# Optimization experiments

Measured on AMD Instinct MI355X. Metric: run time of the kernel, lower is better.

The kernel has to match this reference:

```python
import jax, jax.numpy as jnp
import numpy as np

VOCAB = 32000
EMBED = 512
HIDDEN = 1024
BATCH = 16
SEQ = 256


def setup_inputs() -> dict:
    key = jax.random.key(0)
    ks = jax.random.split(key, 12)
    E, H, V = EMBED, HIDDEN, VOCAB
    s_gate = 1.0 / np.sqrt(E + H)
    s_out = 1.0 / np.sqrt(H)
    return {
        "input": jax.random.randint(ks[0], (BATCH, SEQ), 0, V, dtype=jnp.int32),
        "embed": jax.random.normal(ks[1], (V, E), dtype=jnp.float32),
        "W_f": jax.random.normal(ks[2], (E + H, H), dtype=jnp.float32) * s_gate,
        "b_f": jax.random.normal(ks[3], (H,), dtype=jnp.float32) * s_gate,
        "W_i": jax.random.normal(ks[4], (E + H, H), dtype=jnp.float32) * s_gate,
        "b_i": jax.random.normal(ks[5], (H,), dtype=jnp.float32) * s_gate,
        "W_c": jax.random.normal(ks[6], (E + H, H), dtype=jnp.float32) * s_gate,
        "b_c": jax.random.normal(ks[7], (H,), dtype=jnp.float32) * s_gate,
        "W_o": jax.random.normal(ks[8], (E + H, H), dtype=jnp.float32) * s_gate,
        "b_o": jax.random.normal(ks[9], (H,), dtype=jnp.float32) * s_gate,
        "W_out": jax.random.normal(ks[10], (H, V), dtype=jnp.float32) * s_out,
        "b_out": jax.random.normal(ks[11], (V,), dtype=jnp.float32) * s_out,
    }


def reference(input, embed, W_f, b_f, W_i, b_i, W_c, b_c, W_o, b_o, W_out, b_out):
    B = input.shape[0]
    H = W_f.shape[1]
    tokens = embed[input]                     # [B, S, E]
    xs = jnp.swapaxes(tokens, 0, 1)           # [S, B, E] for scan over time

    def step(carry, x_t):
        h, c = carry
        catted = jnp.concatenate([x_t, h], axis=1)   # [B, E+H]
        f = jax.nn.sigmoid(catted @ W_f + b_f)
        i = jax.nn.sigmoid(catted @ W_i + b_i)
        cand = jnp.tanh(catted @ W_c + b_c)
        o = jax.nn.sigmoid(catted @ W_o + b_o)
        c = c * f + cand * i
        h = c * o
        return (h, c), h

    h0 = jnp.zeros((B, H), dtype=tokens.dtype)
    c0 = jnp.zeros((B, H), dtype=tokens.dtype)
    _, hs = jax.lax.scan(step, (h0, c0), xs)  # hs: [S, B, H]
    hiddens = jnp.swapaxes(hs, 0, 1)          # [B, S, H]
    return hiddens @ W_out + b_out            # [B, S, V]
```

## Files before the change

kernel.cpp:

```cpp
#include <hip/hip_runtime.h>
#include <hip/hip_bf16.h>

#define VOCAB  32000
#define EMBED  512
#define HIDDEN 1024
#define BATCH  16
#define SEQ    256
#define NROW   (BATCH*SEQ)
#define GCOLS  (4*HIDDEN)
#define NWREC  64
#define NWPACK 192
#define NTILE  8000
#define SENT32 0xFFFFFFFFu

typedef unsigned short u16;
typedef unsigned int   u32;
typedef unsigned long long u64;
typedef __attribute__((ext_vector_type(4))) float f32x4;
typedef __attribute__((ext_vector_type(8))) short bf16x8;
typedef __attribute__((ext_vector_type(8))) unsigned short u16x8;
typedef __attribute__((ext_vector_type(2))) unsigned long long u64x2;

__device__ inline u16 f2bf(float f){
  __hip_bfloat16 h = __float2bfloat16(f);
  return __builtin_bit_cast(u16, h);
}
__device__ inline void gload_lds16(const void* g, void* l){
  __builtin_amdgcn_global_load_lds((const __attribute__((address_space(1))) u32*)g,
                                   (__attribute__((address_space(3))) u32*)l, 16, 0, 0);
}
__device__ __forceinline__ u32 al32(const u32* p){
  return __hip_atomic_load(p, __ATOMIC_RELAXED, __HIP_MEMORY_SCOPE_AGENT);
}
__device__ __forceinline__ u64 al64(const u64* p){
  return __hip_atomic_load(p, __ATOMIC_RELAXED, __HIP_MEMORY_SCOPE_AGENT);
}
__device__ __forceinline__ void as32(u32* p, u32 v){
  __hip_atomic_store(p, v, __ATOMIC_RELAXED, __HIP_MEMORY_SCOPE_AGENT);
}
__device__ __forceinline__ void as64(u64* p, u64 v){
  __hip_atomic_store(p, v, __ATOMIC_RELAXED, __HIP_MEMORY_SCOPE_AGENT);
}

__global__ __launch_bounds__(256) void pack_gates(
    const float* __restrict__ Wf, const float* __restrict__ Wi,
    const float* __restrict__ Wc, const float* __restrict__ Wo,
    const float* __restrict__ bf_, const float* __restrict__ bi_,
    const float* __restrict__ bc_, const float* __restrict__ bo_,
    u16* __restrict__ Wxp, u16* __restrict__ Whp, float* __restrict__ bcat)
{
  const int NT_WX = (GCOLS/16)*(EMBED/32)*64;
  const int NT_WH = (GCOLS/16)*(HIDDEN/32)*64;
  int t = blockIdx.x*256 + threadIdx.x;
  if (t < NT_WX){
    int u = t;
    int lane = u&63; int kb = (u>>6)&15; int nblk = u>>10;
    int col = nblk*16 + (lane&15);
    int k0  = kb*32 + ((lane>>4)<<3);
    int g = col>>10, j = col&1023;
    const float* W = (g==0)?Wf:(g==1)?Wi:(g==2)?Wc:Wo;
    u16x8 v;
    #pragma unroll
    for (int e=0;e<8;e++) v[e] = f2bf(W[(size_t)(k0+e)*HIDDEN + j]);
    *(u16x8*)(Wxp + (size_t)u*8) = v;
  } else if (t < NT_WX + NT_WH){
    int u = t - NT_WX;
    int lane = u&63; int kb = (u>>6)&31; int nblk = u>>11;
    int col = nblk*16 + (lane&15);
    int k0  = kb*32 + ((lane>>4)<<3);
    int g = col>>10, j = col&1023;
    const float* W = (g==0)?Wf:(g==1)?Wi:(g==2)?Wc:Wo;
    u16x8 v;
    #pragma unroll
    for (int e=0;e<8;e++) v[e] = f2bf(W[(size_t)(EMBED + k0+e)*HIDDEN + j]);
    *(u16x8*)(Whp + (size_t)u*8) = v;
  } else {
    int u = t - NT_WX - NT_WH;
    if (u < GCOLS){
      int g = u>>10, j = u&1023;
      const float* B = (g==0)?bf_:(g==1)?bi_:(g==2)?bc_:bo_;
      bcat[u] = B[j];
    }
  }
}

__global__ __launch_bounds__(256) void gather_kernel(
    const int* __restrict__ tok, const float* __restrict__ embed, u16* __restrict__ Xg)
{
  int t = blockIdx.x*256 + threadIdx.x;
  int lane = t&63; int kb = (t>>6)&15; int mblk = t>>10;
  int s = mblk; int b = lane&15;
  int token = tok[b*SEQ + s];
  int k0 = kb*32 + ((lane>>4)<<3);
  const float* src = embed + (size_t)token*EMBED + k0;
  u16x8 v;
  #pragma unroll
  for (int e=0;e<8;e++) v[e] = f2bf(src[e]);
  *(u16x8*)(Xg + (size_t)t*8) = v;
}

template<int KB, bool REMAP>
__global__ __launch_bounds__(256,2) void gemm_pk(
    const u16* __restrict__ Ap, const u16* __restrict__ Bp,
    const float* __restrict__ bias, float* __restrict__ C,
    int Nblk128, int N)
{
  __shared__ u16 sm[8192];
  int tid = threadIdx.x; int lane = tid&63; int wv = tid>>6;
  int nwg = gridDim.x;
  int bid = blockIdx.x;
  int swz = (bid&7)*(nwg>>3) + (bid>>3);
  int bm = swz / Nblk128, bn = swz % Nblk128;
  int wr = wv>>1, wc = wv&1;
  f32x4 acc[4][4] = {};
  const u16* Abase = Ap + (size_t)(bm*8)*KB*512;
  const u16* Bbase = Bp + (size_t)(bn*8)*KB*512;
  for (int kb=0; kb<KB; ++kb){
    __syncthreads();
    #pragma unroll
    for (int c2=0;c2<4;c2++){
      int chunk = wv*4 + c2;
      const u16* g;
      if (chunk < 8) g = Abase + ((size_t)chunk*KB + kb)*512 + lane*8;
      else           g = Bbase + ((size_t)(chunk-8)*KB + kb)*512 + lane*8;
      gload_lds16(g, sm + chunk*512);
    }
    __syncthreads();
    bf16x8 a[4], b[4];
    #pragma unroll
    for (int m=0;m<4;m++) a[m] = *(const bf16x8*)(sm + (wr*4+m)*512 + lane*8);
    #pragma unroll
    for (int n=0;n<4;n++) b[n] = *(const bf16x8*)(sm + 4096 + (wc*4+n)*512 + lane*8);
    #pragma unroll
    for (int m=0;m<4;m++)
      #pragma unroll
      for (int n=0;n<4;n++)
        acc[m][n] = __builtin_amdgcn_mfma_f32_16x16x32_bf16(a[m], b[n], acc[m][n], 0,0,0);
  }
  int colb = bn*128 + wc*64;
  int rowb = bm*128 + wr*64;
  #pragma unroll
  for (int m=0;m<4;m++){
    int row0 = rowb + m*16 + (lane>>4)*4;
    #pragma unroll
    for (int n=0;n<4;n++){
      int col = colb + n*16 + (lane&15);
      float bv = bias[col];
      #pragma unroll
      for (int r2=0;r2<4;r2++){
        int row = row0 + r2;
        int orow = REMAP ? ((row&15)*SEQ + (row>>4)) : row;
        C[(size_t)orow*N + col] = acc[m][n][r2] + bv;
      }
    }
  }
}

__global__ __launch_bounds__(256,1) void lstm_fused(
    const u16* __restrict__ Whp, const float* __restrict__ Xpre,
    u16* hb, u16* Hp, u32* cnt, u32* tix, u32* packdone,
    const float* __restrict__ Wout, u16* __restrict__ Woutp,
    const float* __restrict__ bout, float* __restrict__ out)
{
  __shared__ char SMEM[148480];
  __shared__ u32 s_tick;
  u16* smWf = (u16*)SMEM;
  float (*gl)[16][17] = (float (*)[16][17])(SMEM + 131072);
  u16* smg = (u16*)SMEM;

  int tid = threadIdx.x; int lane = tid&63; int v = tid>>6;
  int w = blockIdx.x;

  if (w >= NWREC){
    const int NPK = (VOCAB/16)*(HIDDEN/32)*64;
    int u0 = (w - NWREC)*256 + tid;
    for (int u = u0; u < NPK; u += NWPACK*256){
      int l = u&63; int kb = (u>>6)&31; int nblk = u>>11;
      int col = nblk*16 + (l&15);
      int k0  = kb*32 + ((l>>4)<<3);
      u16x8 vv;
      #pragma unroll
      for (int e=0;e<8;e++) vv[e] = f2bf(Wout[(size_t)(k0+e)*VOCAB + col]);
      u64x2 t2 = __builtin_bit_cast(u64x2, vv);
      u64* dst = (u64*)(Woutp + (size_t)u*8);
      as64(dst+0, t2[0]);
      as64(dst+1, t2[1]);
    }
    asm volatile("s_waitcnt vmcnt(0)" ::: "memory");
    __syncthreads();
    if (tid==0) (void)__hip_atomic_fetch_add(packdone, 1u,
                       __ATOMIC_RELAXED, __HIP_MEMORY_SCOPE_AGENT);
  } else {
    #pragma unroll
    for (int f=0; f<32; ++f){
      int frag = v*32 + f;
      int g = frag>>5, kc = frag&31;
      const u16* src = Whp + ((size_t)(g*64 + w)*32 + kc)*512 + lane*8;
      gload_lds16(src, smWf + (size_t)frag*512);
    }
    asm volatile("s_waitcnt vmcnt(0)" ::: "memory");
    __syncthreads();

    float c = 0.f;
    int pb = tid>>4, pj = tid&15;
    int j = w*16 + pj;
    const int a_row = lane&15, a_k = (lane>>4)*8;
    const float* xb0 = Xpre + (size_t)pb*GCOLS + j;
    float x0 = xb0[0], x1 = xb0[1024], x2 = xb0[2048], x3 = xb0[3072];

    for (int s=0;s<SEQ;s++){
      const u16* rbuf = hb + (size_t)s*16384;
      u64 vv[16];
      for(;;){
        #pragma unroll
        for (int i=0;i<16;i++){
          const u64* p = (const u64*)(rbuf + a_row*1024 + (v*8+(i>>1))*32 + a_k) + (i&1);
          vv[i] = al64(p);
        }
        bool ok = true;
        #pragma unroll
        for (int i=0;i<16;i++)
          ok &= ((u32)vv[i]!=SENT32) & ((u32)(vv[i]>>32)!=SENT32);
        if (ok) break;
        __builtin_amdgcn_s_sleep(1);
      }
      bf16x8 af[8];
      #pragma unroll
      for (int i=0;i<8;i++){
        u64x2 t2 = {vv[2*i], vv[2*i+1]};
        af[i] = __builtin_bit_cast(bf16x8, t2);
      }
      f32x4 acc[4] = {};
      #pragma unroll
      for (int i=0;i<8;i++){
        #pragma unroll
        for (int g=0;g<4;g++){
          bf16x8 wfv = *(const bf16x8*)(smWf + ((size_t)(g*32 + v*8 + i))*512 + lane*8);
          acc[g] = __builtin_amdgcn_mfma_f32_16x16x32_bf16(af[i], wfv, acc[g], 0,0,0);
        }
      }
      {
        int jj = lane&15, b0 = (lane>>4)*4;
        #pragma unroll
        for (int g=0;g<4;g++)
          #pragma unroll
          for (int r2=0;r2<4;r2++)
            gl[v*4+g][b0+r2][jj] = acc[g][r2];
      }
      asm volatile("s_waitcnt lgkmcnt(0)" ::: "memory");
      __builtin_amdgcn_s_barrier();
      __builtin_amdgcn_sched_barrier(0);
      float xn0=0.f,xn1=0.f,xn2=0.f,xn3=0.f;
      if (s < SEQ-1){
        const float* xn = Xpre + ((size_t)(s+1)*16 + pb)*GCOLS + j;
        xn0 = xn[0]; xn1 = xn[1024]; xn2 = xn[2048]; xn3 = xn[3072];
      }
      float p0 = x0 + gl[0][pb][pj] + gl[4][pb][pj] + gl[ 8][pb][pj] + gl[12][pb][pj];
      float p1 = x1 + gl[1][pb][pj] + gl[5][pb][pj] + gl[ 9][pb][pj] + gl[13][pb][pj];
      float p2 = x2 + gl[2][pb][pj] + gl[6][pb][pj] + gl[10][pb][pj] + gl[14][pb][pj];
      float p3 = x3 + gl[3][pb][pj] + gl[7][pb][pj] + gl[11][pb][pj] + gl[15][pb][pj];
      float fg = 1.f/(1.f+__expf(-p0));
      float ig = 1.f/(1.f+__expf(-p1));
      float e2 = __expf(2.f*fminf(fmaxf(p2,-15.f),15.f));
      float cand = (e2-1.f)/(e2+1.f);
      float og = 1.f/(1.f+__expf(-p3));
      c = c*fg + cand*ig;
      float h = c*og;
      x0 = xn0; x1 = xn1; x2 = xn2; x3 = xn3;
      u32 hw_ = (u32)f2bf(h);
      u32 ow_ = (u32)__shfl_xor((int)hw_, 1);
      if ((pj&1)==0){
        u32 word = hw_ | (ow_<<16);
        if (s < SEQ-1){
          u16* wstep = hb + (size_t)(s+1)*16384;
          as32((u32*)wstep + (size_t)pb*512 + w*8 + (pj>>1), word);
        }
        as32((u32*)Hp + (size_t)s*8192 + (size_t)(j>>5)*256
                      + (size_t)(((j>>3)&3)*16 + pb)*4 + ((j&7)>>1), word);
      }
      __builtin_amdgcn_s_barrier();
      __builtin_amdgcn_sched_barrier(0);
      if ((s&7)==7){
        asm volatile("s_waitcnt vmcnt(0)" ::: "memory");
        __builtin_amdgcn_s_barrier();
        asm volatile("" ::: "memory");
        if (tid==0)
          (void)__hip_atomic_fetch_add(cnt + (size_t)(s>>3)*16, 1u,
                   __ATOMIC_RELAXED, __HIP_MEMORY_SCOPE_AGENT);
      }
    }
  }

  if (tid==0){
    while (al32(packdone) < (u32)NWPACK) __builtin_amdgcn_s_sleep(2);
  }
  __syncthreads();

  int wv = tid>>6;
  int wr = wv>>1, wc = wv&1;
  for(;;){
    __syncthreads();
    if (tid==0) s_tick = __hip_atomic_fetch_add(tix, 1u,
                   __ATOMIC_RELAXED, __HIP_MEMORY_SCOPE_AGENT);
    __syncthreads();
    u32 t = s_tick;
    if (t >= (u32)NTILE) break;
    int bm = (int)(t/250u), bn = (int)(t%250u);
    if (tid==0){
      while (al32(cnt + (size_t)bm*16) < (u32)NWREC)
        __builtin_amdgcn_s_sleep(2);
    }
    __syncthreads();
    const u16* Ab = Hp + (size_t)(bm*8)*32*512;
    const u16* Bb = Woutp + (size_t)(bn*8)*32*512;
    auto stage = [&](int kb, int bi){
      #pragma unroll
      for (int c2=0;c2<4;c2++){
        int chunk = wv*4 + c2;
        const u16* g;
        if (chunk < 8) g = Ab + ((size_t)chunk*32 + kb)*512 + lane*8;
        else           g = Bb + ((size_t)(chunk-8)*32 + kb)*512 + lane*8;
        gload_lds16(g, smg + (size_t)bi*8192 + chunk*512);
      }
    };
    stage(0,0); stage(1,1);
    f32x4 acc[4][4] = {};
    for (int kb=0; kb<32; ++kb){
      if (kb<31) asm volatile("s_waitcnt vmcnt(4)" ::: "memory");
      else       asm volatile("s_waitcnt vmcnt(0)" ::: "memory");
      __builtin_amdgcn_s_barrier();
      if (kb+2<32) stage(kb+2, (kb+2)%3);
      const u16* bufp = smg + (size_t)(kb%3)*8192;
      bf16x8 a[4], b[4];
      #pragma unroll
      for (int m=0;m<4;m++) a[m] = *(const bf16x8*)(bufp + (wr*4+m)*512 + lane*8);
      #pragma unroll
      for (int n=0;n<4;n++) b[n] = *(const bf16x8*)(bufp + 4096 + (wc*4+n)*512 + lane*8);
      #pragma unroll
      for (int m=0;m<4;m++)
        #pragma unroll
        for (int n=0;n<4;n++)
          acc[m][n] = __builtin_amdgcn_mfma_f32_16x16x32_bf16(a[m], b[n], acc[m][n], 0,0,0);
    }
    int colb = bn*128 + wc*64;
    int rowb = bm*128 + wr*64;
    #pragma unroll
    for (int m=0;m<4;m++){
      int row0 = rowb + m*16 + (lane>>4)*4;
      #pragma unroll
      for (int n=0;n<4;n++){
        int col = colb + n*16 + (lane&15);
        float bv = bout[col];
        #pragma unroll
        for (int r2=0;r2<4;r2++){
          int row = row0 + r2;
          int orow = (row&15)*SEQ + (row>>4);
          __builtin_nontemporal_store(acc[m][n][r2] + bv,
                                      &out[(size_t)orow*VOCAB + col]);
        }
      }
    }
  }
}

extern "C" void kernel_launch(void* const* d_in, const int* in_sizes, int n_in,
                              void* d_out, int out_size, void* d_ws, size_t ws_size,
                              hipStream_t stream)
{
  (void)in_sizes; (void)n_in; (void)out_size; (void)ws_size;
  const int*   tok   = (const int*)d_in[0];
  const float* embed = (const float*)d_in[1];
  const float* Wf    = (const float*)d_in[2];
  const float* bf_   = (const float*)d_in[3];
  const float* Wi    = (const float*)d_in[4];
  const float* bi_   = (const float*)d_in[5];
  const float* Wc    = (const float*)d_in[6];
  const float* bc_   = (const float*)d_in[7];
  const float* Wo    = (const float*)d_in[8];
  const float* bo_   = (const float*)d_in[9];
  const float* Wout  = (const float*)d_in[10];
  const float* bout  = (const float*)d_in[11];
  float* out = (float*)d_out;

  char* ws = (char*)d_ws;
  size_t off = 0;
  auto alloc = [&](size_t bytes)->void*{
    void* p = ws + off; off += (bytes + 255) & ~(size_t)255; return p;
  };
  u16*  Wxp   = (u16*)alloc((size_t)2097152*2);
  u16*  Xg    = (u16*)alloc((size_t)2097152*2);
  float* bcat = (float*)alloc((size_t)4096*4);
  u16*  hb    = (u16*)ws;
  u16*  Whp   = (u16*)alloc((size_t)4194304*2);
  u16*  Woutp = (u16*)alloc((size_t)32768000*2);
  float* Xpre = (float*)alloc((size_t)NROW*GCOLS*4);
  u16*  Hp    = (u16*)alloc((size_t)4194304*2);
  u32*  cnt   = (u32*)alloc((size_t)4096);
  u32*  tix   = (u32*)alloc((size_t)256);
  u32*  packdone = (u32*)alloc((size_t)256);

  pack_gates<<<3088, 256, 0, stream>>>(Wf,Wi,Wc,Wo, bf_,bi_,bc_,bo_,
                                       Wxp, Whp, bcat);
  gather_kernel<<<1024, 256, 0, stream>>>(tok, embed, Xg);
  gemm_pk<16,false><<<1024, 256, 0, stream>>>(Xg, Wxp, bcat, Xpre, 32, GCOLS);
  (void)hipMemsetAsync(hb, 0x00, 32768, stream);
  (void)hipMemsetAsync((char*)hb + 32768, 0xFF, 255*32768, stream);
  (void)hipMemsetAsync(cnt, 0, 4096 + 256 + 256, stream);
  lstm_fused<<<NWREC+NWPACK, 256, 0, stream>>>(Whp, Xpre, hb, Hp, cnt, tix,
                                               packdone, Wout, Woutp, bout, out);
}
```

Before: 1.169 ms.

## Statically assign output column blocks to worker CTAs and overlap projection with recurrence

Worker CTAs now each own a fixed set of output column tiles (two or one of 250). Each packs only its own Wout slice to bf16 and then computes projection tiles for every row block as soon as the recurrence signals that block done. This removes the global packdone barrier and the atomic ticket dispenser, and the recurrent CTAs no longer join the output GEMM. The projection can overlap with the LSTM recurrence and packed weights are reused locally. The risks are load imbalance between workers with 2 and 1 tiles, and losing the 64 recurrent CTAs as GEMM workers after the recurrence ends.

```diff
diff --git a/kernel.cpp b/kernel.cpp
--- a/kernel.cpp
+++ b/kernel.cpp
@@ -9,8 +9,7 @@
 #define NROW   (BATCH*SEQ)
 #define GCOLS  (4*HIDDEN)
 #define NWREC  64
-#define NWPACK 192
-#define NTILE  8000
+#define NWORK  192
 #define SENT32 0xFFFFFFFFu
 
 typedef unsigned short u16;
@@ -36,9 +35,6 @@
   return __hip_atomic_load(p, __ATOMIC_RELAXED, __HIP_MEMORY_SCOPE_AGENT);
 }
 __device__ __forceinline__ void as32(u32* p, u32 v){
-  __hip_atomic_store(p, v, __ATOMIC_RELAXED, __HIP_MEMORY_SCOPE_AGENT);
-}
-__device__ __forceinline__ void as64(u64* p, u64 v){
   __hip_atomic_store(p, v, __ATOMIC_RELAXED, __HIP_MEMORY_SCOPE_AGENT);
 }
 
@@ -158,12 +154,11 @@
 
 __global__ __launch_bounds__(256,1) void lstm_fused(
     const u16* __restrict__ Whp, const float* __restrict__ Xpre,
-    u16* hb, u16* Hp, u32* cnt, u32* tix, u32* packdone,
+    u16* hb, u16* Hp, u32* cnt,
     const float* __restrict__ Wout, u16* __restrict__ Woutp,
     const float* __restrict__ bout, float* __restrict__ out)
 {
   __shared__ char SMEM[148480];
-  __shared__ u32 s_tick;
   u16* smWf = (u16*)SMEM;
   float (*gl)[16][17] = (float (*)[16][17])(SMEM + 131072);
   u16* smg = (u16*)SMEM;
@@ -172,24 +167,88 @@
   int w = blockIdx.x;
 
   if (w >= NWREC){
-    const int NPK = (VOCAB/16)*(HIDDEN/32)*64;
-    int u0 = (w - NWREC)*256 + tid;
-    for (int u = u0; u < NPK; u += NWPACK*256){
-      int l = u&63; int kb = (u>>6)&31; int nblk = u>>11;
-      int col = nblk*16 + (l&15);
-      int k0  = kb*32 + ((l>>4)<<3);
-      u16x8 vv;
-      #pragma unroll
-      for (int e=0;e<8;e++) vv[e] = f2bf(Wout[(size_t)(k0+e)*VOCAB + col]);
-      u64x2 t2 = __builtin_bit_cast(u64x2, vv);
-      u64* dst = (u64*)(Woutp + (size_t)u*8);
-      as64(dst+0, t2[0]);
-      as64(dst+1, t2[1]);
+    int wkr = w - NWREC;
+    int bn0, nbn;
+    if (wkr < 58){ bn0 = wkr*2;          nbn = 2; }
+    else         { bn0 = 116 + (wkr-58); nbn = 1; }
+    for (int q=0; q<nbn; ++q){
+      int bn = bn0 + q;
+      for (int it = tid; it < 16384; it += 256){
+        int l = it & 63; int kb = (it>>6) & 31; int nb = it >> 11;
+        int nblk = bn*8 + nb;
+        int col = nblk*16 + (l&15);
+        int k0  = kb*32 + ((l>>4)<<3);
+        u16x8 vv;
+        #pragma unroll
+        for (int e=0;e<8;e++) vv[e] = f2bf(Wout[(size_t)(k0+e)*VOCAB + col]);
+        *(u16x8*)(Woutp + ((size_t)(nblk*32 + kb)*64 + l)*8) = vv;
+      }
     }
     asm volatile("s_waitcnt vmcnt(0)" ::: "memory");
     __syncthreads();
-    if (tid==0) (void)__hip_atomic_fetch_add(packdone, 1u,
-                       __ATOMIC_RELAXED, __HIP_MEMORY_SCOPE_AGENT);
+
+    int wv = tid>>6;
+    int wr = wv>>1, wc = wv&1;
+    for (int bm=0; bm<32; ++bm){
+      if (tid==0){
+        while (al32(cnt + (size_t)bm*16) < (u32)NWREC)
+          __builtin_amdgcn_s_sleep(8);
+      }
+      __syncthreads();
+      for (int q=0; q<nbn; ++q){
+        int bn = bn0 + q;
+        const u16* Ab = Hp + (size_t)(bm*8)*32*512;
+        const u16* Bb = Woutp + (size_t)(bn*8)*32*512;
+        auto stage = [&](int kb, int bi){
+          #pragma unroll
+          for (int c2=0;c2<4;c2++){
+            int chunk = wv*4 + c2;
+            const u16* g;
+            if (chunk < 8) g = Ab + ((size_t)chunk*32 + kb)*512 + lane*8;
+            else           g = Bb + ((size_t)(chunk-8)*32 + kb)*512 + lane*8;
+            gload_lds16(g, smg + (size_t)bi*8192 + chunk*512);
+          }
+        };
+        stage(0,0); stage(1,1);
+        f32x4 acc[4][4] = {};
+        for (int kb=0; kb<32; ++kb){
+          if (kb<31) asm volatile("s_waitcnt vmcnt(4)" ::: "memory");
+          else       asm volatile("s_waitcnt vmcnt(0)" ::: "memory");
+          __builtin_amdgcn_s_barrier();
+          if (kb+2<32) stage(kb+2, (kb+2)%3);
+          const u16* bufp = smg + (size_t)(kb%3)*8192;
+          bf16x8 a[4], b[4];
+          #pragma unroll
+          for (int m=0;m<4;m++) a[m] = *(const bf16x8*)(bufp + (wr*4+m)*512 + lane*8);
+          #pragma unroll
+          for (int n=0;n<4;n++) b[n] = *(const bf16x8*)(bufp + 4096 + (wc*4+n)*512 + lane*8);
+          #pragma unroll
+          for (int m=0;m<4;m++)
+            #pragma unroll
+            for (int n=0;n<4;n++)
+              acc[m][n] = __builtin_amdgcn_mfma_f32_16x16x32_bf16(a[m], b[n], acc[m][n], 0,0,0);
+        }
+        int colb = bn*128 + wc*64;
+        int rowb = bm*128 + wr*64;
+        #pragma unroll
+        for (int m=0;m<4;m++){
+          int row0 = rowb + m*16 + (lane>>4)*4;
+          #pragma unroll
+          for (int n=0;n<4;n++){
+            int col = colb + n*16 + (lane&15);
+            float bv = bout[col];
+            #pragma unroll
+            for (int r2=0;r2<4;r2++){
+              int row = row0 + r2;
+              int orow = (row&15)*SEQ + (row>>4);
+              __builtin_nontemporal_store(acc[m][n][r2] + bv,
+                                          &out[(size_t)orow*VOCAB + col]);
+            }
+          }
+        }
+        __syncthreads();
+      }
+    }
   } else {
     #pragma unroll
     for (int f=0; f<32; ++f){
@@ -290,77 +349,6 @@
       }
     }
   }
-
-  if (tid==0){
-    while (al32(packdone) < (u32)NWPACK) __builtin_amdgcn_s_sleep(2);
-  }
-  __syncthreads();
-
-  int wv = tid>>6;
-  int wr = wv>>1, wc = wv&1;
-  for(;;){
-    __syncthreads();
-    if (tid==0) s_tick = __hip_atomic_fetch_add(tix, 1u,
-                   __ATOMIC_RELAXED, __HIP_MEMORY_SCOPE_AGENT);
-    __syncthreads();
-    u32 t = s_tick;
-    if (t >= (u32)NTILE) break;
-    int bm = (int)(t/250u), bn = (int)(t%250u);
-    if (tid==0){
-      while (al32(cnt + (size_t)bm*16) < (u32)NWREC)
-        __builtin_amdgcn_s_sleep(2);
-    }
-    __syncthreads();
-    const u16* Ab = Hp + (size_t)(bm*8)*32*512;
-    const u16* Bb = Woutp + (size_t)(bn*8)*32*512;
-    auto stage = [&](int kb, int bi){
-      #pragma unroll
-      for (int c2=0;c2<4;c2++){
-        int chunk = wv*4 + c2;
-        const u16* g;
-        if (chunk < 8) g = Ab + ((size_t)chunk*32 + kb)*512 + lane*8;
-        else           g = Bb + ((size_t)(chunk-8)*32 + kb)*512 + lane*8;
-        gload_lds16(g, smg + (size_t)bi*8192 + chunk*512);
-      }
-    };
-    stage(0,0); stage(1,1);
-    f32x4 acc[4][4] = {};
-    for (int kb=0; kb<32; ++kb){
-      if (kb<31) asm volatile("s_waitcnt vmcnt(4)" ::: "memory");
-      else       asm volatile("s_waitcnt vmcnt(0)" ::: "memory");
-      __builtin_amdgcn_s_barrier();
-      if (kb+2<32) stage(kb+2, (kb+2)%3);
-      const u16* bufp = smg + (size_t)(kb%3)*8192;
-      bf16x8 a[4], b[4];
-      #pragma unroll
-      for (int m=0;m<4;m++) a[m] = *(const bf16x8*)(bufp + (wr*4+m)*512 + lane*8);
-      #pragma unroll
-      for (int n=0;n<4;n++) b[n] = *(const bf16x8*)(bufp + 4096 + (wc*4+n)*512 + lane*8);
-      #pragma unroll
-      for (int m=0;m<4;m++)
-        #pragma unroll
-        for (int n=0;n<4;n++)
-          acc[m][n] = __builtin_amdgcn_mfma_f32_16x16x32_bf16(a[m], b[n], acc[m][n], 0,0,0);
-    }
-    int colb = bn*128 + wc*64;
-    int rowb = bm*128 + wr*64;
-    #pragma unroll
-    for (int m=0;m<4;m++){
-      int row0 = rowb + m*16 + (lane>>4)*4;
-      #pragma unroll
-      for (int n=0;n<4;n++){
-        int col = colb + n*16 + (lane&15);
-        float bv = bout[col];
-        #pragma unroll
-        for (int r2=0;r2<4;r2++){
-          int row = row0 + r2;
-          int orow = (row&15)*SEQ + (row>>4);
-          __builtin_nontemporal_store(acc[m][n][r2] + bv,
-                                      &out[(size_t)orow*VOCAB + col]);
-        }
-      }
-    }
-  }
 }
 
 extern "C" void kernel_launch(void* const* d_in, const int* in_sizes, int n_in,
@@ -396,8 +384,6 @@
   float* Xpre = (float*)alloc((size_t)NROW*GCOLS*4);
   u16*  Hp    = (u16*)alloc((size_t)4194304*2);
   u32*  cnt   = (u32*)alloc((size_t)4096);
-  u32*  tix   = (u32*)alloc((size_t)256);
-  u32*  packdone = (u32*)alloc((size_t)256);
 
   pack_gates<<<3088, 256, 0, stream>>>(Wf,Wi,Wc,Wo, bf_,bi_,bc_,bo_,
                                        Wxp, Whp, bcat);
@@ -405,7 +391,7 @@
   gemm_pk<16,false><<<1024, 256, 0, stream>>>(Xg, Wxp, bcat, Xpre, 32, GCOLS);
   (void)hipMemsetAsync(hb, 0x00, 32768, stream);
   (void)hipMemsetAsync((char*)hb + 32768, 0xFF, 255*32768, stream);
-  (void)hipMemsetAsync(cnt, 0, 4096 + 256 + 256, stream);
-  lstm_fused<<<NWREC+NWPACK, 256, 0, stream>>>(Whp, Xpre, hb, Hp, cnt, tix,
-                                               packdone, Wout, Woutp, bout, out);
-}
+  (void)hipMemsetAsync(cnt, 0, 4096, stream);
+  lstm_fused<<<NWREC+NWORK, 256, 0, stream>>>(Whp, Xpre, hb, Hp, cnt,
+                                              Wout, Woutp, bout, out);
+}
```

Measured after the change: 1.285 ms. 1.1x slower.
